# Performance work log

Hardware: AMD Instinct MI355X
Metric: run time of the kernel (lower is better)

## Reference

```python
import jax, jax.numpy as jnp
import numpy as np

PRED_LEN = 30
H_DIM = 128
EMB_DIM = 16
DATA_DIM = 2
BATCH = 65536


def setup_inputs() -> dict:
    key = jax.random.key(0)
    ks = jax.random.split(key, 12)
    s = lambda k, shape, scale=1.0: jax.random.normal(k, shape, dtype=jnp.float32) * scale
    return {
        "last_obs": s(ks[0], (BATCH, DATA_DIM)),
        "last_obs_rel": s(ks[1], (BATCH, DATA_DIM)),
        "h0": s(ks[2], (1, BATCH, H_DIM), 0.1),
        "c0": s(ks[3], (1, BATCH, H_DIM), 0.1),
        "W_sp": s(ks[4], (EMB_DIM, DATA_DIM), 0.5),
        "b_sp": s(ks[5], (EMB_DIM,), 0.1),
        "W_ih": s(ks[6], (4 * H_DIM, EMB_DIM), 0.1),
        "b_ih": s(ks[7], (4 * H_DIM,), 0.05),
        "W_hh": s(ks[8], (4 * H_DIM, H_DIM), 0.1),
        "b_hh": s(ks[9], (4 * H_DIM,), 0.05),
        "W_out": s(ks[10], (DATA_DIM, H_DIM), 0.1),
        "b_out": s(ks[11], (DATA_DIM,), 0.05),
    }


def reference(last_obs, last_obs_rel, h0, c0, W_sp, b_sp, W_ih, b_ih, W_hh, b_hh, W_out, b_out):
    # eval mode: dropout is identity. PyTorch LSTM gate order: i, f, g, o.
    h = h0[0]  # (b, H)
    c = c0[0]  # (b, H)
    x = jnp.tanh(last_obs_rel @ W_sp.T + b_sp)  # (b, E)

    def step(carry, _):
        h, c, x = carry
        gates = x @ W_ih.T + b_ih + h @ W_hh.T + b_hh  # (b, 4H)
        i, f, g, o = jnp.split(gates, 4, axis=-1)
        c_new = jax.nn.sigmoid(f) * c + jax.nn.sigmoid(i) * jnp.tanh(g)
        h_new = jax.nn.sigmoid(o) * jnp.tanh(c_new)
        rel_pos = h_new @ W_out.T + b_out  # (b, 2)
        x_new = jnp.tanh(rel_pos @ W_sp.T + b_sp)
        return (h_new, c_new, x_new), rel_pos

    _, traj = jax.lax.scan(step, (h, c, x), None, length=PRED_LEN)  # (T, b, 2)
    return jnp.transpose(traj, (1, 0, 2))  # (b, T, 2)
```

## Files before the change

### kernel.cpp

```cpp
#include <hip/hip_runtime.h>

#define TSTEPS 30
#define KP2 136

#define LOG2E     1.44269504f
#define TWO_LOG2E 2.88539008f

#define SWZ(row, e) ((e) ^ ((((row) >> 3) & 1) << 4))

typedef _Float16 half8 __attribute__((ext_vector_type(8)));
typedef _Float16 half4 __attribute__((ext_vector_type(4)));
typedef float f32x4 __attribute__((ext_vector_type(4)));

#if __has_builtin(__builtin_amdgcn_mfma_f32_16x16x16f16)
#define XK16 1
#else
#define XK16 0
#endif

__device__ __forceinline__ float fexp2(float x) { return __builtin_amdgcn_exp2f(x); }
__device__ __forceinline__ float frcp(float x)  { return __builtin_amdgcn_rcpf(x); }
__device__ __forceinline__ float fsig_pre(float x)  { return frcp(1.0f + fexp2(-x)); }
__device__ __forceinline__ float ftanh_pre(float x) { return 1.0f - 2.0f * frcp(1.0f + fexp2(x)); }

__global__ __launch_bounds__(512, 2)
void lstm30_kernel(const float* __restrict__ last_obs_rel,
                   const float* __restrict__ h0,
                   const float* __restrict__ c0,
                   const float* __restrict__ W_sp,
                   const float* __restrict__ b_sp,
                   const float* __restrict__ W_ih,
                   const float* __restrict__ b_ih,
                   const float* __restrict__ W_hh,
                   const float* __restrict__ b_hh,
                   const float* __restrict__ W_out,
                   const float* __restrict__ b_out,
                   float* __restrict__ out)
{
    __shared__ _Float16 hA[32][KP2];
    __shared__ _Float16 lA[32][KP2];
#if XK16
    __shared__ _Float16 xS[2][16][20];
#else
    __shared__ _Float16 xS[2][16][32];
#endif

    const int tid  = threadIdx.x;
    const int w    = tid >> 6;
    const int L    = tid & 63;
    const int quad = L >> 4;
    const int col  = L & 15;
    const int base = blockIdx.x << 5;

#if XK16
    half8 Wf[4][4];
    half4 Wf4[4];
#else
    half8 Wf[4][5];
#endif
    float bias[4];
    #pragma unroll
    for (int nt = 0; nt < 4; ++nt) {
        const int G = nt * 128 + w * 16 + col;
        const float gsc = (nt == 2) ? TWO_LOG2E : LOG2E;
        bias[nt] = (b_ih[G] + b_hh[G]) * gsc;
        #pragma unroll
        for (int kc = 0; kc < 4; ++kc) {
            const int k0 = kc * 32 + quad * 8;
            const float4 a = *(const float4*)&W_hh[G * 128 + k0];
            const float4 b = *(const float4*)&W_hh[G * 128 + k0 + 4];
            half8 hh;
            hh[0] = (_Float16)(a.x * gsc); hh[1] = (_Float16)(a.y * gsc);
            hh[2] = (_Float16)(a.z * gsc); hh[3] = (_Float16)(a.w * gsc);
            hh[4] = (_Float16)(b.x * gsc); hh[5] = (_Float16)(b.y * gsc);
            hh[6] = (_Float16)(b.z * gsc); hh[7] = (_Float16)(b.w * gsc);
            Wf[nt][kc] = hh;
        }
#if XK16
        {
            const float4 a = *(const float4*)&W_ih[G * 16 + quad * 4];
            half4 h4;
            h4[0] = (_Float16)(a.x * gsc); h4[1] = (_Float16)(a.y * gsc);
            h4[2] = (_Float16)(a.z * gsc); h4[3] = (_Float16)(a.w * gsc);
            Wf4[nt] = h4;
        }
#else
        {
            const int k0 = 128 + quad * 8;
            float v[8];
            if (k0 < 144) {
                const float4 a = *(const float4*)&W_ih[G * 16 + (k0 - 128)];
                const float4 b = *(const float4*)&W_ih[G * 16 + (k0 - 128) + 4];
                v[0]=a.x; v[1]=a.y; v[2]=a.z; v[3]=a.w;
                v[4]=b.x; v[5]=b.y; v[6]=b.z; v[7]=b.w;
            } else {
                #pragma unroll
                for (int jj = 0; jj < 8; ++jj) v[jj] = 0.0f;
            }
            half8 hh;
            #pragma unroll
            for (int jj = 0; jj < 8; ++jj) hh[jj] = (_Float16)(v[jj] * gsc);
            Wf[nt][4] = hh;
        }
#endif
    }

    const float ws0 = W_sp[col * 2 + 0];
    const float ws1 = W_sp[col * 2 + 1];
    const float bs  = b_sp[col];
    const float bo0 = b_out[0], bo1 = b_out[1];

    half8 Ef[4];
    float einit = 0.0f;
    if (w < 4) {
        const bool isM = (w < 2);
        #pragma unroll
        for (int kc = 0; kc < 4; ++kc) {
            const int k0 = kc * 32 + quad * 8;
            const float4 a0 = *(const float4*)&W_out[k0];
            const float4 a1 = *(const float4*)&W_out[k0 + 4];
            const float4 b0 = *(const float4*)&W_out[128 + k0];
            const float4 b1 = *(const float4*)&W_out[128 + k0 + 4];
            float r0[8] = {a0.x,a0.y,a0.z,a0.w,a1.x,a1.y,a1.z,a1.w};
            float r1[8] = {b0.x,b0.y,b0.z,b0.w,b1.x,b1.y,b1.z,b1.w};
            half8 he;
            #pragma unroll
            for (int jj = 0; jj < 8; ++jj)
                he[jj] = isM ? (_Float16)((ws0 * r0[jj] + ws1 * r1[jj]) * TWO_LOG2E)
                             : (_Float16)((col == 0) ? r0[jj] : (col == 1) ? r1[jj] : 0.0f);
            Ef[kc] = he;
        }
        einit = isM ? (ws0 * bo0 + ws1 * bo1 + bs) * TWO_LOG2E
                    : ((col == 0) ? bo0 : (col == 1) ? bo1 : 0.0f);
    }

    float c[2][4];
    #pragma unroll
    for (int tt = 0; tt < 2; ++tt)
        #pragma unroll
        for (int r = 0; r < 4; ++r)
            c[tt][r] = c0[(base + tt * 16 + quad * 4 + r) * 128 + w * 16 + col];

    for (int idx = tid; idx < 32 * 128; idx += 512) {
        const int r = idx >> 7, k = idx & 127;
        const float v = h0[base * 128 + idx];
        const _Float16 hi = (_Float16)v;
        hA[r][SWZ(r, k)] = hi;
        lA[r][SWZ(r, k)] = (_Float16)(v - (float)hi);
    }
    {
        const int rr = tid >> 4;
        const float p0 = last_obs_rel[(base + rr) * 2 + 0];
        const float p1 = last_obs_rel[(base + rr) * 2 + 1];
        xS[rr >> 4][rr & 15][tid & 15] = (_Float16)ftanh_pre(TWO_LOG2E * (ws0 * p0 + ws1 * p1 + bs));
    }
#if !XK16
    for (int flat = tid; flat < 2 * 16 * 16; flat += 512) {
        const int T = flat >> 8, row = (flat >> 4) & 15;
        xS[T][row][16 + (flat & 15)] = (_Float16)0.0f;
    }
#endif
    __syncthreads();

    const int j = w * 16 + col;
    f32x4 accA[4], accB[4];

    for (int k = 0; k < TSTEPS; ++k) {
        {
            half8 a[4];
            #pragma unroll
            for (int kc = 0; kc < 4; ++kc)
                a[kc] = *(const half8*)&hA[col][SWZ(col, kc * 32 + quad * 8)];

            if (k > 0) {
#if XK16
                const half4 xb = *(const half4*)&xS[1][col][quad * 4];
                #pragma unroll
                for (int nt = 0; nt < 4; ++nt)
                    accB[nt] = __builtin_amdgcn_mfma_f32_16x16x16f16(xb, Wf4[nt], accB[nt], 0, 0, 0);
#else
                const half8 xb = *(const half8*)&xS[1][col][quad * 8];
                #pragma unroll
                for (int nt = 0; nt < 4; ++nt)
                    accB[nt] = __builtin_amdgcn_mfma_f32_16x16x32_f16(xb, Wf[nt][4], accB[nt], 0, 0, 0);
#endif
            }

            #pragma unroll
            for (int nt = 0; nt < 4; ++nt) {
                f32x4 bv = {bias[nt], bias[nt], bias[nt], bias[nt]};
                accA[nt] = bv;
            }
            f32x4 eacc = {einit, einit, einit, einit};

            #pragma unroll
            for (int kc = 0; kc < 4; ++kc)
                #pragma unroll
                for (int nt = 0; nt < 4; ++nt)
                    accA[nt] = __builtin_amdgcn_mfma_f32_16x16x32_f16(a[kc], Wf[nt][kc], accA[nt], 0, 0, 0);

            if (k > 0) {
                #pragma unroll
                for (int r = 0; r < 2; ++r) {
                    const int row = 16 + quad * 4 + r;
                    const float gi = fsig_pre(accB[0][r]);
                    const float gf = fsig_pre(accB[1][r]);
                    const float gg = ftanh_pre(accB[2][r]);
                    const float go = fsig_pre(accB[3][r]);
                    c[1][r] = gf * c[1][r] + gi * gg;
                    const float h = go * ftanh_pre(TWO_LOG2E * c[1][r]);
                    const _Float16 hi = (_Float16)h;
                    hA[row][SWZ(row, j)] = hi;
                    lA[row][SWZ(row, j)] = (_Float16)(h - (float)hi);
                }
            }

            if (k > 0 && w == 0) {
                #pragma unroll
                for (int kc = 0; kc < 4; ++kc)
                    eacc = __builtin_amdgcn_mfma_f32_16x16x32_f16(a[kc], Ef[kc], eacc, 0, 0, 0);
            }
            if (k > 0 && w == 2) {
                #pragma unroll
                for (int kc = 0; kc < 4; ++kc)
                    eacc = __builtin_amdgcn_mfma_f32_16x16x32_f16(a[kc], Ef[kc], eacc, 0, 0, 0);
                half8 aL[4];
                #pragma unroll
                for (int kc = 0; kc < 4; ++kc)
                    aL[kc] = *(const half8*)&lA[col][SWZ(col, kc * 32 + quad * 8)];
                #pragma unroll
                for (int kc = 0; kc < 4; ++kc)
                    eacc = __builtin_amdgcn_mfma_f32_16x16x32_f16(aL[kc], Ef[kc], eacc, 0, 0, 0);
            }

            if (k > 0) {
                #pragma unroll
                for (int r = 2; r < 4; ++r) {
                    const int row = 16 + quad * 4 + r;
                    const float gi = fsig_pre(accB[0][r]);
                    const float gf = fsig_pre(accB[1][r]);
                    const float gg = ftanh_pre(accB[2][r]);
                    const float go = fsig_pre(accB[3][r]);
                    c[1][r] = gf * c[1][r] + gi * gg;
                    const float h = go * ftanh_pre(TWO_LOG2E * c[1][r]);
                    const _Float16 hi = (_Float16)h;
                    hA[row][SWZ(row, j)] = hi;
                    lA[row][SWZ(row, j)] = (_Float16)(h - (float)hi);
                }
            }

            if (k > 0 && w == 0) {
                #pragma unroll
                for (int r = 0; r < 4; ++r)
                    xS[0][quad * 4 + r][col] = (_Float16)ftanh_pre(eacc[r]);
            }
            if (k > 0 && w == 2 && col < 2) {
                #pragma unroll
                for (int r = 0; r < 4; ++r)
                    out[(base + quad * 4 + r) * (TSTEPS * 2) + (k - 1) * 2 + col] = eacc[r];
            }
            __syncthreads();
        }
        {
            half8 a[4];
            #pragma unroll
            for (int kc = 0; kc < 4; ++kc)
                a[kc] = *(const half8*)&hA[16 + col][SWZ(16 + col, kc * 32 + quad * 8)];

            {
#if XK16
                const half4 xa = *(const half4*)&xS[0][col][quad * 4];
                #pragma unroll
                for (int nt = 0; nt < 4; ++nt)
                    accA[nt] = __builtin_amdgcn_mfma_f32_16x16x16f16(xa, Wf4[nt], accA[nt], 0, 0, 0);
#else
                const half8 xa = *(const half8*)&xS[0][col][quad * 8];
                #pragma unroll
                for (int nt = 0; nt < 4; ++nt)
                    accA[nt] = __builtin_amdgcn_mfma_f32_16x16x32_f16(xa, Wf[nt][4], accA[nt], 0, 0, 0);
#endif
            }

            #pragma unroll
            for (int nt = 0; nt < 4; ++nt) {
                f32x4 bv = {bias[nt], bias[nt], bias[nt], bias[nt]};
                accB[nt] = bv;
            }
            f32x4 eacc = {einit, einit, einit, einit};

            #pragma unroll
            for (int kc = 0; kc < 4; ++kc)
                #pragma unroll
                for (int nt = 0; nt < 4; ++nt)
                    accB[nt] = __builtin_amdgcn_mfma_f32_16x16x32_f16(a[kc], Wf[nt][kc], accB[nt], 0, 0, 0);

            {
                #pragma unroll
                for (int r = 0; r < 2; ++r) {
                    const int row = quad * 4 + r;
                    const float gi = fsig_pre(accA[0][r]);
                    const float gf = fsig_pre(accA[1][r]);
                    const float gg = ftanh_pre(accA[2][r]);
                    const float go = fsig_pre(accA[3][r]);
                    c[0][r] = gf * c[0][r] + gi * gg;
                    const float h = go * ftanh_pre(TWO_LOG2E * c[0][r]);
                    const _Float16 hi = (_Float16)h;
                    hA[row][SWZ(row, j)] = hi;
                    lA[row][SWZ(row, j)] = (_Float16)(h - (float)hi);
                }
            }

            if (w == 1) {
                #pragma unroll
                for (int kc = 0; kc < 4; ++kc)
                    eacc = __builtin_amdgcn_mfma_f32_16x16x32_f16(a[kc], Ef[kc], eacc, 0, 0, 0);
            }
            if (w == 3) {
                #pragma unroll
                for (int kc = 0; kc < 4; ++kc)
                    eacc = __builtin_amdgcn_mfma_f32_16x16x32_f16(a[kc], Ef[kc], eacc, 0, 0, 0);
                half8 aL[4];
                #pragma unroll
                for (int kc = 0; kc < 4; ++kc)
                    aL[kc] = *(const half8*)&lA[16 + col][SWZ(16 + col, kc * 32 + quad * 8)];
                #pragma unroll
                for (int kc = 0; kc < 4; ++kc)
                    eacc = __builtin_amdgcn_mfma_f32_16x16x32_f16(aL[kc], Ef[kc], eacc, 0, 0, 0);
            }

            {
                #pragma unroll
                for (int r = 2; r < 4; ++r) {
                    const int row = quad * 4 + r;
                    const float gi = fsig_pre(accA[0][r]);
                    const float gf = fsig_pre(accA[1][r]);
                    const float gg = ftanh_pre(accA[2][r]);
                    const float go = fsig_pre(accA[3][r]);
                    c[0][r] = gf * c[0][r] + gi * gg;
                    const float h = go * ftanh_pre(TWO_LOG2E * c[0][r]);
                    const _Float16 hi = (_Float16)h;
                    hA[row][SWZ(row, j)] = hi;
                    lA[row][SWZ(row, j)] = (_Float16)(h - (float)hi);
                }
            }

            if (k > 0 && w == 1) {
                #pragma unroll
                for (int r = 0; r < 4; ++r)
                    xS[1][quad * 4 + r][col] = (_Float16)ftanh_pre(eacc[r]);
            }
            if (k > 0 && w == 3 && col < 2) {
                #pragma unroll
                for (int r = 0; r < 4; ++r)
                    out[(base + 16 + quad * 4 + r) * (TSTEPS * 2) + (k - 1) * 2 + col] = eacc[r];
            }
            __syncthreads();
        }
    }

    {
        {
#if XK16
            const half4 xb = *(const half4*)&xS[1][col][quad * 4];
            #pragma unroll
            for (int nt = 0; nt < 4; ++nt)
                accB[nt] = __builtin_amdgcn_mfma_f32_16x16x16f16(xb, Wf4[nt], accB[nt], 0, 0, 0);
#else
            const half8 xb = *(const half8*)&xS[1][col][quad * 8];
            #pragma unroll
            for (int nt = 0; nt < 4; ++nt)
                accB[nt] = __builtin_amdgcn_mfma_f32_16x16x32_f16(xb, Wf[nt][4], accB[nt], 0, 0, 0);
#endif
        }
        if (w == 2) {
            f32x4 eacc = {einit, einit, einit, einit};
            #pragma unroll
            for (int kc = 0; kc < 4; ++kc) {
                const half8 aH = *(const half8*)&hA[col][SWZ(col, kc * 32 + quad * 8)];
                eacc = __builtin_amdgcn_mfma_f32_16x16x32_f16(aH, Ef[kc], eacc, 0, 0, 0);
            }
            #pragma unroll
            for (int kc = 0; kc < 4; ++kc) {
                const half8 aL = *(const half8*)&lA[col][SWZ(col, kc * 32 + quad * 8)];
                eacc = __builtin_amdgcn_mfma_f32_16x16x32_f16(aL, Ef[kc], eacc, 0, 0, 0);
            }
            if (col < 2) {
                #pragma unroll
                for (int r = 0; r < 4; ++r)
                    out[(base + quad * 4 + r) * (TSTEPS * 2) + (TSTEPS - 1) * 2 + col] = eacc[r];
            }
        }
        #pragma unroll
        for (int r = 0; r < 4; ++r) {
            const int row = 16 + quad * 4 + r;
            const float gi = fsig_pre(accB[0][r]);
            const float gf = fsig_pre(accB[1][r]);
            const float gg = ftanh_pre(accB[2][r]);
            const float go = fsig_pre(accB[3][r]);
            c[1][r] = gf * c[1][r] + gi * gg;
            const float h = go * ftanh_pre(TWO_LOG2E * c[1][r]);
            const _Float16 hi = (_Float16)h;
            hA[row][SWZ(row, j)] = hi;
            lA[row][SWZ(row, j)] = (_Float16)(h - (float)hi);
        }
        __syncthreads();
        if (w == 3) {
            f32x4 eacc = {einit, einit, einit, einit};
            #pragma unroll
            for (int kc = 0; kc < 4; ++kc) {
                const half8 aH = *(const half8*)&hA[16 + col][SWZ(16 + col, kc * 32 + quad * 8)];
                eacc = __builtin_amdgcn_mfma_f32_16x16x32_f16(aH, Ef[kc], eacc, 0, 0, 0);
            }
            #pragma unroll
            for (int kc = 0; kc < 4; ++kc) {
                const half8 aL = *(const half8*)&lA[16 + col][SWZ(16 + col, kc * 32 + quad * 8)];
                eacc = __builtin_amdgcn_mfma_f32_16x16x32_f16(aL, Ef[kc], eacc, 0, 0, 0);
            }
            if (col < 2) {
                #pragma unroll
                for (int r = 0; r < 4; ++r)
                    out[(base + 16 + quad * 4 + r) * (TSTEPS * 2) + (TSTEPS - 1) * 2 + col] = eacc[r];
            }
        }
    }
}

extern "C" void kernel_launch(void* const* d_in, const int* in_sizes, int n_in,
                              void* d_out, int out_size, void* d_ws, size_t ws_size,
                              hipStream_t stream) {
    const float* last_obs_rel = (const float*)d_in[1];
    const float* h0    = (const float*)d_in[2];
    const float* c0    = (const float*)d_in[3];
    const float* W_sp  = (const float*)d_in[4];
    const float* b_sp  = (const float*)d_in[5];
    const float* W_ih  = (const float*)d_in[6];
    const float* b_ih  = (const float*)d_in[7];
    const float* W_hh  = (const float*)d_in[8];
    const float* b_hh  = (const float*)d_in[9];
    const float* W_out = (const float*)d_in[10];
    const float* b_out = (const float*)d_in[11];
    float* out = (float*)d_out;

    const int batch = in_sizes[2] / 128;
    lstm30_kernel<<<dim3(batch / 32), dim3(512), 0, stream>>>(
        last_obs_rel, h0, c0, W_sp, b_sp, W_ih, b_ih, W_hh, b_hh, W_out, b_out, out);
}
```

Before: 627.1 us.

## Process 128 rows per block with double-buffered hidden state and staggered tile groups

Each block now handles 128 batch rows (8 tiles of 16) instead of 32, with the hidden state double-buffered across steps. Tiles are split into two groups whose timesteps are staggered, so the output-projection and embedding work for one group overlaps the LSTM step of the other, with two barriers per step. Each phase runs two independent MFMA chains to hide latency. Weight loading is amortised over more rows and there are fewer blocks. In exchange, LDS use and register pressure (c[8][4], dual accumulators) rise, occupancy may fall, and the h0 low-part buffer is no longer initialised.

Result: faster. 540.1 us (-13.9%).

```diff
diff --git a/kernel.cpp b/kernel.cpp
--- a/kernel.cpp
+++ b/kernel.cpp
@@ -2,6 +2,7 @@
 
 #define TSTEPS 30
 #define KP2 136
+#define NROWS 128
 
 #define LOG2E     1.44269504f
 #define TWO_LOG2E 2.88539008f
@@ -22,6 +23,109 @@
 __device__ __forceinline__ float frcp(float x)  { return __builtin_amdgcn_rcpf(x); }
 __device__ __forceinline__ float fsig_pre(float x)  { return frcp(1.0f + fexp2(-x)); }
 __device__ __forceinline__ float ftanh_pre(float x) { return 1.0f - 2.0f * frcp(1.0f + fexp2(x)); }
+
+#define CELL_ROW(ACC, CC, TT, R) do {                                   \
+    const float gi_ = fsig_pre(ACC[0][R]);                              \
+    const float gf_ = fsig_pre(ACC[1][R]);                              \
+    const float gg_ = ftanh_pre(ACC[2][R]);                             \
+    const float go_ = fsig_pre(ACC[3][R]);                              \
+    CC = gf_ * CC + gi_ * gg_;                                          \
+    const float hv_ = go_ * ftanh_pre(TWO_LOG2E * CC);                  \
+    const _Float16 hh_ = (_Float16)hv_;                                 \
+    const int row_ = (TT) * 16 + quad * 4 + (R);                        \
+    hP[wpl][row_][SWZ(row_, j)] = hh_;                                  \
+    lP[row_][SWZ(row_, j)] = (_Float16)(hv_ - (float)hh_);              \
+} while (0)
+
+#if XK16
+#define XFIN(TA, TB) do {                                               \
+    const half4 xa_ = *(const half4*)&xS[TA][col][quad * 4];            \
+    const half4 xb_ = *(const half4*)&xS[TB][col][quad * 4];            \
+    _Pragma("unroll")                                                   \
+    for (int nt = 0; nt < 4; ++nt) {                                    \
+        accA[nt] = __builtin_amdgcn_mfma_f32_16x16x16f16(xa_, Wf4[nt], accA[nt], 0, 0, 0); \
+        accB[nt] = __builtin_amdgcn_mfma_f32_16x16x16f16(xb_, Wf4[nt], accB[nt], 0, 0, 0); \
+    }                                                                   \
+} while (0)
+#else
+#define XFIN(TA, TB) do {                                               \
+    const half8 xa_ = *(const half8*)&xS[TA][col][quad * 8];            \
+    const half8 xb_ = *(const half8*)&xS[TB][col][quad * 8];            \
+    _Pragma("unroll")                                                   \
+    for (int nt = 0; nt < 4; ++nt) {                                    \
+        accA[nt] = __builtin_amdgcn_mfma_f32_16x16x32_f16(xa_, Wf[nt][4], accA[nt], 0, 0, 0); \
+        accB[nt] = __builtin_amdgcn_mfma_f32_16x16x32_f16(xb_, Wf[nt][4], accB[nt], 0, 0, 0); \
+    }                                                                   \
+} while (0)
+#endif
+
+#define EJOB_X(ET, EPL) do {                                            \
+    f32x4 eacc = {einit, einit, einit, einit};                          \
+    _Pragma("unroll")                                                   \
+    for (int kc = 0; kc < 4; ++kc) {                                    \
+        const half8 aH_ = *(const half8*)&hP[EPL][(ET) * 16 + col][SWZ((ET) * 16 + col, kc * 32 + quad * 8)]; \
+        eacc = __builtin_amdgcn_mfma_f32_16x16x32_f16(aH_, Ef[kc], eacc, 0, 0, 0); \
+    }                                                                   \
+    _Pragma("unroll")                                                   \
+    for (int r = 0; r < 4; ++r)                                         \
+        xS[ET][quad * 4 + r][col] = (_Float16)ftanh_pre(eacc[r]);       \
+} while (0)
+
+#define EJOB_REL(ET, KEV, EPL) do {                                     \
+    f32x4 eacc = {einit, einit, einit, einit};                          \
+    _Pragma("unroll")                                                   \
+    for (int kc = 0; kc < 4; ++kc) {                                    \
+        const half8 aH_ = *(const half8*)&hP[EPL][(ET) * 16 + col][SWZ((ET) * 16 + col, kc * 32 + quad * 8)]; \
+        eacc = __builtin_amdgcn_mfma_f32_16x16x32_f16(aH_, Ef[kc], eacc, 0, 0, 0); \
+    }                                                                   \
+    _Pragma("unroll")                                                   \
+    for (int kc = 0; kc < 4; ++kc) {                                    \
+        const half8 aL_ = *(const half8*)&lP[(ET) * 16 + col][SWZ((ET) * 16 + col, kc * 32 + quad * 8)]; \
+        eacc = __builtin_amdgcn_mfma_f32_16x16x32_f16(aL_, Ef[kc], eacc, 0, 0, 0); \
+    }                                                                   \
+    if (col < 2) {                                                      \
+        _Pragma("unroll")                                               \
+        for (int r = 0; r < 4; ++r)                                     \
+            out[(base + (ET) * 16 + quad * 4 + r) * (TSTEPS * 2) + (KEV) * 2 + col] = eacc[r]; \
+    }                                                                   \
+} while (0)
+
+#define PHASE(TA, TB, EA, EB, DOE, KEV, EPL) do {                       \
+    if (doStep) {                                                       \
+        half8 aA[4], aB[4];                                             \
+        _Pragma("unroll")                                               \
+        for (int kc = 0; kc < 4; ++kc) {                                \
+            aA[kc] = *(const half8*)&hP[rpl][(TA) * 16 + col][SWZ((TA) * 16 + col, kc * 32 + quad * 8)]; \
+            aB[kc] = *(const half8*)&hP[rpl][(TB) * 16 + col][SWZ((TB) * 16 + col, kc * 32 + quad * 8)]; \
+        }                                                               \
+        _Pragma("unroll")                                               \
+        for (int nt = 0; nt < 4; ++nt) {                                \
+            f32x4 bv = {bias[nt], bias[nt], bias[nt], bias[nt]};        \
+            accA[nt] = bv; accB[nt] = bv;                               \
+        }                                                               \
+        XFIN(TA, TB);                                                   \
+        _Pragma("unroll")                                               \
+        for (int kc = 0; kc < 4; ++kc)                                  \
+            _Pragma("unroll")                                           \
+            for (int nt = 0; nt < 4; ++nt) {                            \
+                accA[nt] = __builtin_amdgcn_mfma_f32_16x16x32_f16(aA[kc], Wf[nt][kc], accA[nt], 0, 0, 0); \
+                accB[nt] = __builtin_amdgcn_mfma_f32_16x16x32_f16(aB[kc], Wf[nt][kc], accB[nt], 0, 0, 0); \
+            }                                                           \
+    }                                                                   \
+    if (DOE) {                                                          \
+        if (w == 0 && (KEV) < TSTEPS - 1) EJOB_X(EA, EPL);              \
+        if (w == 1 && (KEV) < TSTEPS - 1) EJOB_X(EB, EPL);              \
+        if (w == 2) EJOB_REL(EA, KEV, EPL);                             \
+        if (w == 3) EJOB_REL(EB, KEV, EPL);                             \
+    }                                                                   \
+    if (doStep) {                                                       \
+        _Pragma("unroll")                                               \
+        for (int r = 0; r < 4; ++r) {                                   \
+            CELL_ROW(accA, c[TA][r], TA, r);                            \
+            CELL_ROW(accB, c[TB][r], TB, r);                            \
+        }                                                               \
+    }                                                                   \
+} while (0)
 
 __global__ __launch_bounds__(512, 2)
 void lstm30_kernel(const float* __restrict__ last_obs_rel,
@@ -37,12 +141,12 @@
                    const float* __restrict__ b_out,
                    float* __restrict__ out)
 {
-    __shared__ _Float16 hA[32][KP2];
-    __shared__ _Float16 lA[32][KP2];
+    __shared__ _Float16 hP[2][NROWS][KP2];
+    __shared__ _Float16 lP[NROWS][KP2];
 #if XK16
-    __shared__ _Float16 xS[2][16][20];
-#else
-    __shared__ _Float16 xS[2][16][32];
+    __shared__ _Float16 xS[8][16][20];
+#else
+    __shared__ _Float16 xS[8][16][32];
 #endif
 
     const int tid  = threadIdx.x;
@@ -50,7 +154,7 @@
     const int L    = tid & 63;
     const int quad = L >> 4;
     const int col  = L & 15;
-    const int base = blockIdx.x << 5;
+    const int base = blockIdx.x << 7;
 
 #if XK16
     half8 Wf[4][4];
@@ -111,9 +215,9 @@
     const float bo0 = b_out[0], bo1 = b_out[1];
 
     half8 Ef[4];
-    float einit = 0.0f;
-    if (w < 4) {
-        const bool isM = (w < 2);
+    float einit;
+    {
+        const bool isM = ((w & 2) == 0);
         #pragma unroll
         for (int kc = 0; kc < 4; ++kc) {
             const int k0 = kc * 32 + quad * 8;
@@ -134,294 +238,52 @@
                     : ((col == 0) ? bo0 : (col == 1) ? bo1 : 0.0f);
     }
 
-    float c[2][4];
+    const int j = w * 16 + col;
+
+    float c[8][4];
     #pragma unroll
-    for (int tt = 0; tt < 2; ++tt)
+    for (int t = 0; t < 8; ++t)
         #pragma unroll
         for (int r = 0; r < 4; ++r)
-            c[tt][r] = c0[(base + tt * 16 + quad * 4 + r) * 128 + w * 16 + col];
-
-    for (int idx = tid; idx < 32 * 128; idx += 512) {
-        const int r = idx >> 7, k = idx & 127;
-        const float v = h0[base * 128 + idx];
-        const _Float16 hi = (_Float16)v;
-        hA[r][SWZ(r, k)] = hi;
-        lA[r][SWZ(r, k)] = (_Float16)(v - (float)hi);
-    }
-    {
-        const int rr = tid >> 4;
+            c[t][r] = c0[(base + t * 16 + quad * 4 + r) * 128 + j];
+
+    for (int i = tid; i < NROWS * 32; i += 512) {
+        const int r  = i >> 5;
+        const int k4 = (i & 31) * 4;
+        const float4 v = *(const float4*)&h0[(base + r) * 128 + k4];
+        half4 hv;
+        hv[0] = (_Float16)v.x; hv[1] = (_Float16)v.y;
+        hv[2] = (_Float16)v.z; hv[3] = (_Float16)v.w;
+        *(half4*)&hP[1][r][SWZ(r, k4)] = hv;
+    }
+    #pragma unroll
+    for (int hh = 0; hh < 4; ++hh) {
+        const int rr = (tid >> 4) + hh * 32;
         const float p0 = last_obs_rel[(base + rr) * 2 + 0];
         const float p1 = last_obs_rel[(base + rr) * 2 + 1];
-        xS[rr >> 4][rr & 15][tid & 15] = (_Float16)ftanh_pre(TWO_LOG2E * (ws0 * p0 + ws1 * p1 + bs));
+        xS[rr >> 4][rr & 15][col] = (_Float16)ftanh_pre(TWO_LOG2E * (ws0 * p0 + ws1 * p1 + bs));
     }
 #if !XK16
-    for (int flat = tid; flat < 2 * 16 * 16; flat += 512) {
-        const int T = flat >> 8, row = (flat >> 4) & 15;
-        xS[T][row][16 + (flat & 15)] = (_Float16)0.0f;
+    for (int flat = tid; flat < 8 * 16 * 16; flat += 512) {
+        xS[flat >> 8][(flat >> 4) & 15][16 + (flat & 15)] = (_Float16)0.0f;
     }
 #endif
     __syncthreads();
 
-    const int j = w * 16 + col;
-    f32x4 accA[4], accB[4];
-
-    for (int k = 0; k < TSTEPS; ++k) {
-        {
-            half8 a[4];
-            #pragma unroll
-            for (int kc = 0; kc < 4; ++kc)
-                a[kc] = *(const half8*)&hA[col][SWZ(col, kc * 32 + quad * 8)];
-
-            if (k > 0) {
-#if XK16
-                const half4 xb = *(const half4*)&xS[1][col][quad * 4];
-                #pragma unroll
-                for (int nt = 0; nt < 4; ++nt)
-                    accB[nt] = __builtin_amdgcn_mfma_f32_16x16x16f16(xb, Wf4[nt], accB[nt], 0, 0, 0);
-#else
-                const half8 xb = *(const half8*)&xS[1][col][quad * 8];
-                #pragma unroll
-                for (int nt = 0; nt < 4; ++nt)
-                    accB[nt] = __builtin_amdgcn_mfma_f32_16x16x32_f16(xb, Wf[nt][4], accB[nt], 0, 0, 0);
-#endif
-            }
-
-            #pragma unroll
-            for (int nt = 0; nt < 4; ++nt) {
-                f32x4 bv = {bias[nt], bias[nt], bias[nt], bias[nt]};
-                accA[nt] = bv;
-            }
-            f32x4 eacc = {einit, einit, einit, einit};
-
-            #pragma unroll
-            for (int kc = 0; kc < 4; ++kc)
-                #pragma unroll
-                for (int nt = 0; nt < 4; ++nt)
-                    accA[nt] = __builtin_amdgcn_mfma_f32_16x16x32_f16(a[kc], Wf[nt][kc], accA[nt], 0, 0, 0);
-
-            if (k > 0) {
-                #pragma unroll
-                for (int r = 0; r < 2; ++r) {
-                    const int row = 16 + quad * 4 + r;
-                    const float gi = fsig_pre(accB[0][r]);
-                    const float gf = fsig_pre(accB[1][r]);
-                    const float gg = ftanh_pre(accB[2][r]);
-                    const float go = fsig_pre(accB[3][r]);
-                    c[1][r] = gf * c[1][r] + gi * gg;
-                    const float h = go * ftanh_pre(TWO_LOG2E * c[1][r]);
-                    const _Float16 hi = (_Float16)h;
-                    hA[row][SWZ(row, j)] = hi;
-                    lA[row][SWZ(row, j)] = (_Float16)(h - (float)hi);
-                }
-            }
-
-            if (k > 0 && w == 0) {
-                #pragma unroll
-                for (int kc = 0; kc < 4; ++kc)
-                    eacc = __builtin_amdgcn_mfma_f32_16x16x32_f16(a[kc], Ef[kc], eacc, 0, 0, 0);
-            }
-            if (k > 0 && w == 2) {
-                #pragma unroll
-                for (int kc = 0; kc < 4; ++kc)
-                    eacc = __builtin_amdgcn_mfma_f32_16x16x32_f16(a[kc], Ef[kc], eacc, 0, 0, 0);
-                half8 aL[4];
-                #pragma unroll
-                for (int kc = 0; kc < 4; ++kc)
-                    aL[kc] = *(const half8*)&lA[col][SWZ(col, kc * 32 + quad * 8)];
-                #pragma unroll
-                for (int kc = 0; kc < 4; ++kc)
-                    eacc = __builtin_amdgcn_mfma_f32_16x16x32_f16(aL[kc], Ef[kc], eacc, 0, 0, 0);
-            }
-
-            if (k > 0) {
-                #pragma unroll
-                for (int r = 2; r < 4; ++r) {
-                    const int row = 16 + quad * 4 + r;
-                    const float gi = fsig_pre(accB[0][r]);
-                    const float gf = fsig_pre(accB[1][r]);
-                    const float gg = ftanh_pre(accB[2][r]);
-                    const float go = fsig_pre(accB[3][r]);
-                    c[1][r] = gf * c[1][r] + gi * gg;
-                    const float h = go * ftanh_pre(TWO_LOG2E * c[1][r]);
-                    const _Float16 hi = (_Float16)h;
-                    hA[row][SWZ(row, j)] = hi;
-                    lA[row][SWZ(row, j)] = (_Float16)(h - (float)hi);
-                }
-            }
-
-            if (k > 0 && w == 0) {
-                #pragma unroll
-                for (int r = 0; r < 4; ++r)
-                    xS[0][quad * 4 + r][col] = (_Float16)ftanh_pre(eacc[r]);
-            }
-            if (k > 0 && w == 2 && col < 2) {
-                #pragma unroll
-                for (int r = 0; r < 4; ++r)
-                    out[(base + quad * 4 + r) * (TSTEPS * 2) + (k - 1) * 2 + col] = eacc[r];
-            }
-            __syncthreads();
-        }
-        {
-            half8 a[4];
-            #pragma unroll
-            for (int kc = 0; kc < 4; ++kc)
-                a[kc] = *(const half8*)&hA[16 + col][SWZ(16 + col, kc * 32 + quad * 8)];
-
-            {
-#if XK16
-                const half4 xa = *(const half4*)&xS[0][col][quad * 4];
-                #pragma unroll
-                for (int nt = 0; nt < 4; ++nt)
-                    accA[nt] = __builtin_amdgcn_mfma_f32_16x16x16f16(xa, Wf4[nt], accA[nt], 0, 0, 0);
-#else
-                const half8 xa = *(const half8*)&xS[0][col][quad * 8];
-                #pragma unroll
-                for (int nt = 0; nt < 4; ++nt)
-                    accA[nt] = __builtin_amdgcn_mfma_f32_16x16x32_f16(xa, Wf[nt][4], accA[nt], 0, 0, 0);
-#endif
-            }
-
-            #pragma unroll
-            for (int nt = 0; nt < 4; ++nt) {
-                f32x4 bv = {bias[nt], bias[nt], bias[nt], bias[nt]};
-                accB[nt] = bv;
-            }
-            f32x4 eacc = {einit, einit, einit, einit};
-
-            #pragma unroll
-            for (int kc = 0; kc < 4; ++kc)
-                #pragma unroll
-                for (int nt = 0; nt < 4; ++nt)
-                    accB[nt] = __builtin_amdgcn_mfma_f32_16x16x32_f16(a[kc], Wf[nt][kc], accB[nt], 0, 0, 0);
-
-            {
-                #pragma unroll
-                for (int r = 0; r < 2; ++r) {
-                    const int row = quad * 4 + r;
-                    const float gi = fsig_pre(accA[0][r]);
-                    const float gf = fsig_pre(accA[1][r]);
-                    const float gg = ftanh_pre(accA[2][r]);
-                    const float go = fsig_pre(accA[3][r]);
-                    c[0][r] = gf * c[0][r] + gi * gg;
-                    const float h = go * ftanh_pre(TWO_LOG2E * c[0][r]);
-                    const _Float16 hi = (_Float16)h;
-                    hA[row][SWZ(row, j)] = hi;
-                    lA[row][SWZ(row, j)] = (_Float16)(h - (float)hi);
-                }
-            }
-
-            if (w == 1) {
-                #pragma unroll
-                for (int kc = 0; kc < 4; ++kc)
-                    eacc = __builtin_amdgcn_mfma_f32_16x16x32_f16(a[kc], Ef[kc], eacc, 0, 0, 0);
-            }
-            if (w == 3) {
-                #pragma unroll
-                for (int kc = 0; kc < 4; ++kc)
-                    eacc = __builtin_amdgcn_mfma_f32_16x16x32_f16(a[kc], Ef[kc], eacc, 0, 0, 0);
-                half8 aL[4];
-                #pragma unroll
-                for (int kc = 0; kc < 4; ++kc)
-                    aL[kc] = *(const half8*)&lA[16 + col][SWZ(16 + col, kc * 32 + quad * 8)];
-                #pragma unroll
-                for (int kc = 0; kc < 4; ++kc)
-                    eacc = __builtin_amdgcn_mfma_f32_16x16x32_f16(aL[kc], Ef[kc], eacc, 0, 0, 0);
-            }
-
-            {
-                #pragma unroll
-                for (int r = 2; r < 4; ++r) {
-                    const int row = quad * 4 + r;
-                    const float gi = fsig_pre(accA[0][r]);
-                    const float gf = fsig_pre(accA[1][r]);
-                    const float gg = ftanh_pre(accA[2][r]);
-                    const float go = fsig_pre(accA[3][r]);
-                    c[0][r] = gf * c[0][r] + gi * gg;
-                    const float h = go * ftanh_pre(TWO_LOG2E * c[0][r]);
-                    const _Float16 hi = (_Float16)h;
-                    hA[row][SWZ(row, j)] = hi;
-                    lA[row][SWZ(row, j)] = (_Float16)(h - (float)hi);
-                }
-            }
-
-            if (k > 0 && w == 1) {
-                #pragma unroll
-                for (int r = 0; r < 4; ++r)
-                    xS[1][quad * 4 + r][col] = (_Float16)ftanh_pre(eacc[r]);
-            }
-            if (k > 0 && w == 3 && col < 2) {
-                #pragma unroll
-                for (int r = 0; r < 4; ++r)
-                    out[(base + 16 + quad * 4 + r) * (TSTEPS * 2) + (k - 1) * 2 + col] = eacc[r];
-            }
-            __syncthreads();
-        }
-    }
-
-    {
-        {
-#if XK16
-            const half4 xb = *(const half4*)&xS[1][col][quad * 4];
-            #pragma unroll
-            for (int nt = 0; nt < 4; ++nt)
-                accB[nt] = __builtin_amdgcn_mfma_f32_16x16x16f16(xb, Wf4[nt], accB[nt], 0, 0, 0);
-#else
-            const half8 xb = *(const half8*)&xS[1][col][quad * 8];
-            #pragma unroll
-            for (int nt = 0; nt < 4; ++nt)
-                accB[nt] = __builtin_amdgcn_mfma_f32_16x16x32_f16(xb, Wf[nt][4], accB[nt], 0, 0, 0);
-#endif
-        }
-        if (w == 2) {
-            f32x4 eacc = {einit, einit, einit, einit};
-            #pragma unroll
-            for (int kc = 0; kc < 4; ++kc) {
-                const half8 aH = *(const half8*)&hA[col][SWZ(col, kc * 32 + quad * 8)];
-                eacc = __builtin_amdgcn_mfma_f32_16x16x32_f16(aH, Ef[kc], eacc, 0, 0, 0);
-            }
-            #pragma unroll
-            for (int kc = 0; kc < 4; ++kc) {
-                const half8 aL = *(const half8*)&lA[col][SWZ(col, kc * 32 + quad * 8)];
-                eacc = __builtin_amdgcn_mfma_f32_16x16x32_f16(aL, Ef[kc], eacc, 0, 0, 0);
-            }
-            if (col < 2) {
-                #pragma unroll
-                for (int r = 0; r < 4; ++r)
-                    out[(base + quad * 4 + r) * (TSTEPS * 2) + (TSTEPS - 1) * 2 + col] = eacc[r];
-            }
-        }
-        #pragma unroll
-        for (int r = 0; r < 4; ++r) {
-            const int row = 16 + quad * 4 + r;
-            const float gi = fsig_pre(accB[0][r]);
-            const float gf = fsig_pre(accB[1][r]);
-            const float gg = ftanh_pre(accB[2][r]);
-            const float go = fsig_pre(accB[3][r]);
-            c[1][r] = gf * c[1][r] + gi * gg;
-            const float h = go * ftanh_pre(TWO_LOG2E * c[1][r]);
-            const _Float16 hi = (_Float16)h;
-            hA[row][SWZ(row, j)] = hi;
-            lA[row][SWZ(row, j)] = (_Float16)(h - (float)hi);
-        }
+    for (int kk = 0; kk <= TSTEPS; ++kk) {
+        const int wpl = kk & 1;
+        const int rpl = wpl ^ 1;
+        const bool doStep = (kk < TSTEPS);
+        const bool doE01  = (kk >= 1);
+        const bool doE23  = (kk < TSTEPS);
+        f32x4 accA[4], accB[4];
+
+        PHASE(0, 1, 4, 5, doE01, kk - 1, rpl);
+        PHASE(2, 3, 6, 7, doE01, kk - 1, rpl);
         __syncthreads();
-        if (w == 3) {
-            f32x4 eacc = {einit, einit, einit, einit};
-            #pragma unroll
-            for (int kc = 0; kc < 4; ++kc) {
-                const half8 aH = *(const half8*)&hA[16 + col][SWZ(16 + col, kc * 32 + quad * 8)];
-                eacc = __builtin_amdgcn_mfma_f32_16x16x32_f16(aH, Ef[kc], eacc, 0, 0, 0);
-            }
-            #pragma unroll
-            for (int kc = 0; kc < 4; ++kc) {
-                const half8 aL = *(const half8*)&lA[16 + col][SWZ(16 + col, kc * 32 + quad * 8)];
-                eacc = __builtin_amdgcn_mfma_f32_16x16x32_f16(aL, Ef[kc], eacc, 0, 0, 0);
-            }
-            if (col < 2) {
-                #pragma unroll
-                for (int r = 0; r < 4; ++r)
-                    out[(base + 16 + quad * 4 + r) * (TSTEPS * 2) + (TSTEPS - 1) * 2 + col] = eacc[r];
-            }
-        }
+        PHASE(4, 5, 0, 1, doE23, kk, wpl);
+        PHASE(6, 7, 2, 3, doE23, kk, wpl);
+        __syncthreads();
     }
 }
 
@@ -442,6 +304,6 @@
     float* out = (float*)d_out;
 
     const int batch = in_sizes[2] / 128;
-    lstm30_kernel<<<dim3(batch / 32), dim3(512), 0, stream>>>(
+    lstm30_kernel<<<dim3(batch / 128), dim3(512), 0, stream>>>(
         last_obs_rel, h0, c0, W_sp, b_sp, W_ih, b_ih, W_hh, b_hh, W_out, b_out, out);
 }
```
